# Optimization experiments

Hardware: AMD Instinct MI355X
Metric: run time of the kernel (lower is better)

## Reference

```python
import jax, jax.numpy as jnp
import numpy as np


def setup_inputs() -> dict:
    key = jax.random.key(0)
    k1, k2 = jax.random.split(key)
    x = jax.random.normal(k1, (16, 8192, 128), dtype=jnp.float32)
    embed = jax.random.normal(k2, (1024, 128), dtype=jnp.float32)
    return {"x": x, "embed": embed}


def reference(x, embed):
    # preprocess: flatten leading dims -> (N, d)
    shape = x.shape
    xf = x.reshape(-1, shape[-1])  # (N, d)
    # quantize: negative squared Euclidean distance, argmax over codebook
    dist = (2.0 * (xf @ embed.T)
            - jnp.sum(xf * xf, axis=1, keepdims=True)
            - jnp.sum(embed * embed, axis=1)[None, :])
    embed_ind = jnp.argmax(dist, axis=-1)  # (N,)
    # postprocess indices back to input leading shape
    embed_ind = embed_ind.reshape(shape[:-1])
    # dequantize: embedding lookup
    quantize = embed[embed_ind]  # (..., d)
    return embed_ind, quantize
```

## Files before the change

kernel.cpp:

```cpp
#include <hip/hip_runtime.h>
#include <math.h>


typedef __attribute__((ext_vector_type(8)))  short short8_t;
typedef __attribute__((ext_vector_type(16))) float floatx16;

constexpr int D        = 128;
constexpr int KCODES   = 1024;
constexpr int NTILES   = 32;
constexpr int NPAIRS   = 16;
constexpr int ROWS_BLK = 128;
constexpr float TAU    = 0.015f;

constexpr size_t WS_NCSQ = 0;
constexpr size_t WS_EHI  = 4096;
constexpr size_t WS_ELO  = WS_EHI + 262144;

#define GLOBAL_AS __attribute__((address_space(1)))
#define LDS_AS    __attribute__((address_space(3)))

__device__ inline unsigned short bf16_rne(float v, float* back) {
    unsigned u = __float_as_uint(v);
    unsigned r = (u + 0x7FFFu + ((u >> 16) & 1u)) >> 16;
    *back = __uint_as_float(r << 16);
    return (unsigned short)r;
}

__global__ __launch_bounds__(256)
void ecb_prep(const float* __restrict__ embed, float* __restrict__ ncsq,
              unsigned short* __restrict__ ehi, unsigned short* __restrict__ elo) {
    const int tid = threadIdx.x;
    const int cc = tid & 15;
    const int nl = tid >> 4;
    const int n  = blockIdx.x * 16 + nl;
    const int t = n >> 5, nn = n & 31;
    const float* src = embed + (size_t)n * D + cc * 8;
    float4 a = *(const float4*)src;
    float4 b = *(const float4*)(src + 4);
    float vv[8] = {a.x, a.y, a.z, a.w, b.x, b.y, b.z, b.w};
    float ss = 0.f;
    unsigned short hq[8], lq[8];
#pragma unroll
    for (int j = 0; j < 8; ++j) {
        ss = fmaf(vv[j], vv[j], ss);
        float hb, db;
        hq[j] = bf16_rne(vv[j], &hb);
        lq[j] = bf16_rne(vv[j] - hb, &db);
    }
    uint4 ph, pl;
    ph.x = (unsigned)hq[0] | ((unsigned)hq[1] << 16);
    ph.y = (unsigned)hq[2] | ((unsigned)hq[3] << 16);
    ph.z = (unsigned)hq[4] | ((unsigned)hq[5] << 16);
    ph.w = (unsigned)hq[6] | ((unsigned)hq[7] << 16);
    pl.x = (unsigned)lq[0] | ((unsigned)lq[1] << 16);
    pl.y = (unsigned)lq[2] | ((unsigned)lq[3] << 16);
    pl.z = (unsigned)lq[4] | ((unsigned)lq[5] << 16);
    pl.w = (unsigned)lq[6] | ((unsigned)lq[7] << 16);
    size_t dst = ((size_t)(t * 8 + (cc >> 1)) * 64 + (size_t)((cc & 1) * 32 + nn)) * 8;
    *(uint4*)(ehi + dst) = ph;
    *(uint4*)(elo + dst) = pl;
#pragma unroll
    for (int m = 1; m < 16; m <<= 1) ss += __shfl_xor(ss, m, 64);
    if (cc == 0) ncsq[n] = -ss;
}

__global__ __launch_bounds__(256, 2)
void ecb_main(const float* __restrict__ x,
              const unsigned short* __restrict__ ehi, const unsigned short* __restrict__ elo,
              const float* __restrict__ ncsq, const float* __restrict__ embed,
              float* __restrict__ out_idx, float* __restrict__ out_q) {
    __shared__ short8_t ebuf[2][2][2][512];
    __shared__ float ncsq_s[KCODES];
    __shared__ int   sidx[ROWS_BLK];
    __shared__ unsigned char llist[ROWS_BLK];
    __shared__ unsigned lcount;

    const int tid  = threadIdx.x;
    const int lane = tid & 63, wave = tid >> 6;
    const int col  = lane & 31, h = lane >> 5;
    const long rowblk = (long)blockIdx.x * ROWS_BLK;
    const int  roww   = wave * 32;

    if (tid == 0) lcount = 0u;

    auto stage = [&](int p, int bb) {
#pragma unroll
        for (int tt = 0; tt < 2; ++tt) {
            const char* gh = (const char*)ehi + (size_t)(2 * p + tt) * 8192;
            const char* gl = (const char*)elo + (size_t)(2 * p + tt) * 8192;
            char* lh = (char*)&ebuf[bb][tt][0][0];
            char* ll = (char*)&ebuf[bb][tt][1][0];
            const int off = wave * 2048;
            __builtin_amdgcn_global_load_lds((const GLOBAL_AS unsigned int*)(gh + off + lane * 16),
                                             (LDS_AS unsigned int*)(lh + off), 16, 0, 0);
            __builtin_amdgcn_global_load_lds((const GLOBAL_AS unsigned int*)(gh + off + 1024 + lane * 16),
                                             (LDS_AS unsigned int*)(lh + off + 1024), 16, 0, 0);
            __builtin_amdgcn_global_load_lds((const GLOBAL_AS unsigned int*)(gl + off + lane * 16),
                                             (LDS_AS unsigned int*)(ll + off), 16, 0, 0);
            __builtin_amdgcn_global_load_lds((const GLOBAL_AS unsigned int*)(gl + off + 1024 + lane * 16),
                                             (LDS_AS unsigned int*)(ll + off + 1024), 16, 0, 0);
        }
    };

    stage(0, 0);
    ((float4*)ncsq_s)[tid] = ((const float4*)ncsq)[tid];

    short8_t ah[8], al[8];
    {
        const float* xr = x + (rowblk + roww + col) * (long)D + h * 8;
#pragma unroll
        for (int c = 0; c < 8; ++c) {
            float4 a  = *(const float4*)(xr + c * 16);
            float4 b  = *(const float4*)(xr + c * 16 + 4);
            float vv[8] = {a.x, a.y, a.z, a.w, b.x, b.y, b.z, b.w};
            short8_t fh, fl;
#pragma unroll
            for (int j = 0; j < 8; ++j) {
                float v2x = vv[j] + vv[j];
                float hb, db;
                fh[j] = (short)bf16_rne(v2x, &hb);
                fl[j] = (short)bf16_rne(v2x - hb, &db);
            }
            ah[c] = fh;
            al[c] = fl;
        }
    }

    float v1[16], v2[16];
#pragma unroll
    for (int j = 0; j < 16; ++j) { v1[j] = -INFINITY; v2[j] = -INFINITY; }

    __syncthreads();

#pragma unroll 1
    for (int p = 0; p < NPAIRS; ++p) {
        const int b = p & 1;
        if (p + 1 < NPAIRS) stage(p + 1, b ^ 1);

#pragma unroll
        for (int tt = 0; tt < 2; ++tt) {
            const int t = 2 * p + tt;
            const float negcs = ncsq_s[t * 32 + col];

            floatx16 accA, accB;
#pragma unroll
            for (int i = 0; i < 16; ++i) { accA[i] = negcs; accB[i] = 0.f; }

#pragma unroll
            for (int s = 0; s < 8; ++s) {
                short8_t bh = ebuf[b][tt][0][s * 64 + lane];
                short8_t bl = ebuf[b][tt][1][s * 64 + lane];
                accA = __builtin_amdgcn_mfma_f32_32x32x16_bf16(ah[s], bh, accA, 0, 0, 0);
                accB = __builtin_amdgcn_mfma_f32_32x32x16_bf16(al[s], bh, accB, 0, 0, 0);
                accB = __builtin_amdgcn_mfma_f32_32x32x16_bf16(ah[s], bl, accB, 0, 0, 0);
            }

#pragma unroll
            for (int j = 0; j < 16; ++j) {
                float sc = accA[j] + accB[j];
                unsigned u = (__float_as_uint(sc) & ~31u) | (unsigned)t;
                float cand = __uint_as_float(u);
                float vo = v1[j];
                v1[j] = fmaxf(vo, cand);
                v2[j] = __builtin_amdgcn_fmed3f(vo, v2[j], cand);
            }
        }
        __syncthreads();
    }

#pragma unroll
    for (int j = 0; j < 16; ++j) {
        float a1 = v1[j], a2 = v2[j];
        int   c1 = (int)((__float_as_uint(a1) & 31u) << 5) | col;
#pragma unroll
        for (int m = 1; m < 32; m <<= 1) {
            float o1 = __shfl_xor(a1, m, 64);
            int   oc = __shfl_xor(c1, m, 64);
            float o2 = __shfl_xor(a2, m, 64);
            float lo = fminf(a1, o1);
            if (o1 > a1) { a1 = o1; c1 = oc; }
            a2 = fmaxf(fmaxf(a2, o2), lo);
        }
        if (col == j) {
            int row_local = roww + (j & 3) + 8 * (j >> 2) + 4 * h;
            sidx[row_local] = c1;
            out_idx[rowblk + row_local] = (float)c1;
            if (a1 - a2 < TAU) {
                unsigned p2 = atomicAdd(&lcount, 1u);
                llist[p2] = (unsigned char)row_local;
            }
        }
    }
    __syncthreads();

    for (int i = tid; i < ROWS_BLK * 32; i += 256) {
        int r = i >> 5, q = i & 31;
        int code = sidx[r];
        float4 ev = *(const float4*)(embed + (size_t)code * D + q * 4);
        *(float4*)(out_q + (rowblk + r) * (long)D + q * 4) = ev;
    }
    __syncthreads();

    float* xs = (float*)&ebuf[0][0][0][0];
    float* bv = xs + D;
    int*   bi = (int*)(bv + 256);
    const unsigned nf = lcount;
    for (unsigned f = 0; f < nf; ++f) {
        const int rl  = llist[f];
        const long row = rowblk + rl;
        if (tid < 32) *(float4*)&xs[tid * 4] = *(const float4*)(x + row * D + tid * 4);
        __syncthreads();
        const int c0 = tid * 4;
        float s0 = 0.f, s1 = 0.f, s2 = 0.f, s3 = 0.f;
#pragma unroll 4
        for (int kc = 0; kc < 32; ++kc) {
            float4 xv = *(const float4*)&xs[kc * 4];
            float4 e0 = *(const float4*)(embed + (size_t)(c0 + 0) * D + kc * 4);
            float4 e1 = *(const float4*)(embed + (size_t)(c0 + 1) * D + kc * 4);
            float4 e2 = *(const float4*)(embed + (size_t)(c0 + 2) * D + kc * 4);
            float4 e3 = *(const float4*)(embed + (size_t)(c0 + 3) * D + kc * 4);
            s0 = fmaf(xv.x, e0.x, s0); s0 = fmaf(xv.y, e0.y, s0);
            s0 = fmaf(xv.z, e0.z, s0); s0 = fmaf(xv.w, e0.w, s0);
            s1 = fmaf(xv.x, e1.x, s1); s1 = fmaf(xv.y, e1.y, s1);
            s1 = fmaf(xv.z, e1.z, s1); s1 = fmaf(xv.w, e1.w, s1);
            s2 = fmaf(xv.x, e2.x, s2); s2 = fmaf(xv.y, e2.y, s2);
            s2 = fmaf(xv.z, e2.z, s2); s2 = fmaf(xv.w, e2.w, s2);
            s3 = fmaf(xv.x, e3.x, s3); s3 = fmaf(xv.y, e3.y, s3);
            s3 = fmaf(xv.z, e3.z, s3); s3 = fmaf(xv.w, e3.w, s3);
        }
        float scs[4] = {fmaf(2.f, s0, ncsq_s[c0]),
                        fmaf(2.f, s1, ncsq_s[c0 + 1]),
                        fmaf(2.f, s2, ncsq_s[c0 + 2]),
                        fmaf(2.f, s3, ncsq_s[c0 + 3])};
        float best = -INFINITY; int bidx = 0;
#pragma unroll
        for (int i = 0; i < 4; ++i)
            if (scs[i] > best) { best = scs[i]; bidx = c0 + i; }
        bv[tid] = best; bi[tid] = bidx;
        __syncthreads();
        for (int s = 128; s > 0; s >>= 1) {
            if (tid < s) {
                float ov = bv[tid + s]; int oi = bi[tid + s];
                if (ov > bv[tid] || (ov == bv[tid] && oi < bi[tid])) { bv[tid] = ov; bi[tid] = oi; }
            }
            __syncthreads();
        }
        const int win = bi[0];
        if (tid == 0) out_idx[row] = (float)win;
        if (tid < 32) {
            float4 ev = *(const float4*)(embed + (size_t)win * D + tid * 4);
            *(float4*)(out_q + row * D + tid * 4) = ev;
        }
        __syncthreads();
    }
}

extern "C" void kernel_launch(void* const* d_in, const int* in_sizes, int n_in,
                              void* d_out, int out_size, void* d_ws, size_t ws_size,
                              hipStream_t stream) {
    const float* x     = (const float*)d_in[0];
    const float* embed = (const float*)d_in[1];
    const int N = in_sizes[0] / D;
    char* ws = (char*)d_ws;
    float*          ncsq = (float*)(ws + WS_NCSQ);
    unsigned short* ehi  = (unsigned short*)(ws + WS_EHI);
    unsigned short* elo  = (unsigned short*)(ws + WS_ELO);
    float* out_idx = (float*)d_out;
    float* out_q   = out_idx + N;

    hipLaunchKernelGGL(ecb_prep, dim3(64), dim3(256), 0, stream,
                       embed, ncsq, ehi, elo);
    hipLaunchKernelGGL(ecb_main, dim3(N / ROWS_BLK), dim3(256), 0, stream,
                       x, ehi, elo, ncsq, embed, out_idx, out_q);
}
```

Measured before the change: 281.9 us.

## Use XOR-swizzled codebook layout with single-tile staging and higher occupancy

Changes the prepared bf16 codebook layout to row-major per code with an XOR swizzle on 16-byte chunks, and reads B fragments from LDS with the matching swizzle to avoid bank conflicts. Staging now double-buffers one 32-code tile per iteration instead of pairs, which shrinks LDS and drops the shared ncsq copy (ncsq is read from global). This lets launch bounds target 3 blocks per CU. The factor of two moves from the x split into an fma on the accumulator, and the cost is one barrier per tile instead of per pair.

```diff
diff --git a/kernel.cpp b/kernel.cpp
--- a/kernel.cpp
+++ b/kernel.cpp
@@ -8,7 +8,6 @@
 constexpr int D        = 128;
 constexpr int KCODES   = 1024;
 constexpr int NTILES   = 32;
-constexpr int NPAIRS   = 16;
 constexpr int ROWS_BLK = 128;
 constexpr float TAU    = 0.015f;
 
@@ -33,7 +32,7 @@
     const int cc = tid & 15;
     const int nl = tid >> 4;
     const int n  = blockIdx.x * 16 + nl;
-    const int t = n >> 5, nn = n & 31;
+    const int t = n >> 5, nn = n & 31, nm = nn & 15;
     const float* src = embed + (size_t)n * D + cc * 8;
     float4 a = *(const float4*)src;
     float4 b = *(const float4*)(src + 4);
@@ -56,7 +55,8 @@
     pl.y = (unsigned)lq[2] | ((unsigned)lq[3] << 16);
     pl.z = (unsigned)lq[4] | ((unsigned)lq[5] << 16);
     pl.w = (unsigned)lq[6] | ((unsigned)lq[7] << 16);
-    size_t dst = ((size_t)(t * 8 + (cc >> 1)) * 64 + (size_t)((cc & 1) * 32 + nn)) * 8;
+    const size_t tb = (size_t)t * 32 * D + (size_t)nn * D;
+    size_t dst = tb + (size_t)(((cc ^ nm)) * 8);
     *(uint4*)(ehi + dst) = ph;
     *(uint4*)(elo + dst) = pl;
 #pragma unroll
@@ -64,46 +64,23 @@
     if (cc == 0) ncsq[n] = -ss;
 }
 
-__global__ __launch_bounds__(256, 2)
+__global__ __launch_bounds__(256, 3)
 void ecb_main(const float* __restrict__ x,
               const unsigned short* __restrict__ ehi, const unsigned short* __restrict__ elo,
               const float* __restrict__ ncsq, const float* __restrict__ embed,
               float* __restrict__ out_idx, float* __restrict__ out_q) {
-    __shared__ short8_t ebuf[2][2][2][512];
-    __shared__ float ncsq_s[KCODES];
-    __shared__ int   sidx[ROWS_BLK];
+    __shared__ unsigned short ebuf[2][2][4096];
+    __shared__ int sidx[ROWS_BLK];
     __shared__ unsigned char llist[ROWS_BLK];
     __shared__ unsigned lcount;
 
     const int tid  = threadIdx.x;
     const int lane = tid & 63, wave = tid >> 6;
-    const int col  = lane & 31, h = lane >> 5;
+    const int col  = lane & 31, h = lane >> 5, colm = col & 15;
     const long rowblk = (long)blockIdx.x * ROWS_BLK;
     const int  roww   = wave * 32;
 
     if (tid == 0) lcount = 0u;
-
-    auto stage = [&](int p, int bb) {
-#pragma unroll
-        for (int tt = 0; tt < 2; ++tt) {
-            const char* gh = (const char*)ehi + (size_t)(2 * p + tt) * 8192;
-            const char* gl = (const char*)elo + (size_t)(2 * p + tt) * 8192;
-            char* lh = (char*)&ebuf[bb][tt][0][0];
-            char* ll = (char*)&ebuf[bb][tt][1][0];
-            const int off = wave * 2048;
-            __builtin_amdgcn_global_load_lds((const GLOBAL_AS unsigned int*)(gh + off + lane * 16),
-                                             (LDS_AS unsigned int*)(lh + off), 16, 0, 0);
-            __builtin_amdgcn_global_load_lds((const GLOBAL_AS unsigned int*)(gh + off + 1024 + lane * 16),
-                                             (LDS_AS unsigned int*)(lh + off + 1024), 16, 0, 0);
-            __builtin_amdgcn_global_load_lds((const GLOBAL_AS unsigned int*)(gl + off + lane * 16),
-                                             (LDS_AS unsigned int*)(ll + off), 16, 0, 0);
-            __builtin_amdgcn_global_load_lds((const GLOBAL_AS unsigned int*)(gl + off + 1024 + lane * 16),
-                                             (LDS_AS unsigned int*)(ll + off + 1024), 16, 0, 0);
-        }
-    };
-
-    stage(0, 0);
-    ((float4*)ncsq_s)[tid] = ((const float4*)ncsq)[tid];
 
     short8_t ah[8], al[8];
     {
@@ -111,59 +88,72 @@
 #pragma unroll
         for (int c = 0; c < 8; ++c) {
             float4 a  = *(const float4*)(xr + c * 16);
-            float4 b  = *(const float4*)(xr + c * 16 + 4);
-            float vv[8] = {a.x, a.y, a.z, a.w, b.x, b.y, b.z, b.w};
+            float4 bq = *(const float4*)(xr + c * 16 + 4);
+            float vv[8] = {a.x, a.y, a.z, a.w, bq.x, bq.y, bq.z, bq.w};
             short8_t fh, fl;
 #pragma unroll
             for (int j = 0; j < 8; ++j) {
-                float v2x = vv[j] + vv[j];
                 float hb, db;
-                fh[j] = (short)bf16_rne(v2x, &hb);
-                fl[j] = (short)bf16_rne(v2x - hb, &db);
+                fh[j] = (short)bf16_rne(vv[j], &hb);
+                fl[j] = (short)bf16_rne(vv[j] - hb, &db);
             }
             ah[c] = fh;
             al[c] = fl;
         }
     }
 
+    auto stage = [&](int t, int b) {
+        const char* gh = (const char*)(ehi) + (size_t)t * 8192;
+        const char* gl = (const char*)(elo) + (size_t)t * 8192;
+        char* lh = (char*)&ebuf[b][0][0];
+        char* ll = (char*)&ebuf[b][1][0];
+#pragma unroll
+        for (int i = 0; i < 2; ++i) {
+            int off = i * 4096 + wave * 1024;
+            __builtin_amdgcn_global_load_lds((const GLOBAL_AS unsigned int*)(gh + off + lane * 16),
+                                             (LDS_AS unsigned int*)(lh + off), 16, 0, 0);
+            __builtin_amdgcn_global_load_lds((const GLOBAL_AS unsigned int*)(gl + off + lane * 16),
+                                             (LDS_AS unsigned int*)(ll + off), 16, 0, 0);
+        }
+    };
+
     float v1[16], v2[16];
 #pragma unroll
     for (int j = 0; j < 16; ++j) { v1[j] = -INFINITY; v2[j] = -INFINITY; }
 
+    stage(0, 0);
     __syncthreads();
 
 #pragma unroll 1
-    for (int p = 0; p < NPAIRS; ++p) {
-        const int b = p & 1;
-        if (p + 1 < NPAIRS) stage(p + 1, b ^ 1);
-
-#pragma unroll
-        for (int tt = 0; tt < 2; ++tt) {
-            const int t = 2 * p + tt;
-            const float negcs = ncsq_s[t * 32 + col];
-
-            floatx16 accA, accB;
-#pragma unroll
-            for (int i = 0; i < 16; ++i) { accA[i] = negcs; accB[i] = 0.f; }
-
-#pragma unroll
-            for (int s = 0; s < 8; ++s) {
-                short8_t bh = ebuf[b][tt][0][s * 64 + lane];
-                short8_t bl = ebuf[b][tt][1][s * 64 + lane];
-                accA = __builtin_amdgcn_mfma_f32_32x32x16_bf16(ah[s], bh, accA, 0, 0, 0);
-                accB = __builtin_amdgcn_mfma_f32_32x32x16_bf16(al[s], bh, accB, 0, 0, 0);
-                accB = __builtin_amdgcn_mfma_f32_32x32x16_bf16(ah[s], bl, accB, 0, 0, 0);
-            }
-
-#pragma unroll
-            for (int j = 0; j < 16; ++j) {
-                float sc = accA[j] + accB[j];
-                unsigned u = (__float_as_uint(sc) & ~31u) | (unsigned)t;
-                float cand = __uint_as_float(u);
-                float vo = v1[j];
-                v1[j] = fmaxf(vo, cand);
-                v2[j] = __builtin_amdgcn_fmed3f(vo, v2[j], cand);
-            }
+    for (int t = 0; t < NTILES; ++t) {
+        const int b = t & 1;
+        if (t + 1 < NTILES) stage(t + 1, (t + 1) & 1);
+
+        const float negcs = ncsq[t * 32 + col];
+
+        floatx16 accA, accB;
+#pragma unroll
+        for (int i = 0; i < 16; ++i) { accA[i] = 0.f; accB[i] = 0.f; }
+
+#pragma unroll
+        for (int s = 0; s < 8; ++s) {
+            const int cc = 2 * s + h;
+            const int idx = (col * 16 + (cc ^ colm)) * 8;
+            short8_t bh = *(const short8_t*)&ebuf[b][0][idx];
+            short8_t bl = *(const short8_t*)&ebuf[b][1][idx];
+            accA = __builtin_amdgcn_mfma_f32_32x32x16_bf16(ah[s], bh, accA, 0, 0, 0);
+            accB = __builtin_amdgcn_mfma_f32_32x32x16_bf16(al[s], bh, accB, 0, 0, 0);
+            accB = __builtin_amdgcn_mfma_f32_32x32x16_bf16(ah[s], bl, accB, 0, 0, 0);
+        }
+
+#pragma unroll
+        for (int j = 0; j < 16; ++j) {
+            float sc = fmaf(2.f, accA[j] + accB[j], negcs);
+            unsigned u = (__float_as_uint(sc) & ~31u) | (unsigned)t;
+            float cand = __uint_as_float(u);
+            float vo = v1[j];
+            v1[j] = fmaxf(vo, cand);
+            v2[j] = __builtin_amdgcn_fmed3f(vo, v2[j], cand);
         }
         __syncthreads();
     }
@@ -186,8 +176,8 @@
             sidx[row_local] = c1;
             out_idx[rowblk + row_local] = (float)c1;
             if (a1 - a2 < TAU) {
-                unsigned p2 = atomicAdd(&lcount, 1u);
-                llist[p2] = (unsigned char)row_local;
+                unsigned p = atomicAdd(&lcount, 1u);
+                llist[p] = (unsigned char)row_local;
             }
         }
     }
@@ -201,7 +191,7 @@
     }
     __syncthreads();
 
-    float* xs = (float*)&ebuf[0][0][0][0];
+    float* xs = (float*)&ebuf[0][0][0];
     float* bv = xs + D;
     int*   bi = (int*)(bv + 256);
     const unsigned nf = lcount;
@@ -228,10 +218,9 @@
             s3 = fmaf(xv.x, e3.x, s3); s3 = fmaf(xv.y, e3.y, s3);
             s3 = fmaf(xv.z, e3.z, s3); s3 = fmaf(xv.w, e3.w, s3);
         }
-        float scs[4] = {fmaf(2.f, s0, ncsq_s[c0]),
-                        fmaf(2.f, s1, ncsq_s[c0 + 1]),
-                        fmaf(2.f, s2, ncsq_s[c0 + 2]),
-                        fmaf(2.f, s3, ncsq_s[c0 + 3])};
+        float4 nc = *(const float4*)(ncsq + c0);
+        float scs[4] = {fmaf(2.f, s0, nc.x), fmaf(2.f, s1, nc.y),
+                        fmaf(2.f, s2, nc.z), fmaf(2.f, s3, nc.w)};
         float best = -INFINITY; int bidx = 0;
 #pragma unroll
         for (int i = 0; i < 4; ++i)
```

Measured after the change: 294.9 us. 4.6% more time.
